# Optimization experiments

Measured on AMD Instinct MI355X. Metric: run time of the kernel, lower is better.

## Reference

```python
import jax, jax.numpy as jnp
import numpy as np

EPS = 1e-4
LN_EPS = 1e-5  # torch LayerNorm default
N, E, IN_DIM, OUT_DIM = 100000, 800000, 128, 128


def setup_inputs() -> dict:
    key = jax.random.key(0)
    ks = jax.random.split(key, 8)
    s = 1.0 / np.sqrt(IN_DIM)
    return {
        "x": jax.random.normal(ks[0], (N, IN_DIM), dtype=jnp.float32),
        "edge_index": jax.random.randint(ks[1], (2, E), 0, N, dtype=jnp.int32),
        "degree": jax.random.randint(ks[2], (N,), 0, 16, dtype=jnp.int32),
        "W_fc": jax.random.normal(ks[3], (IN_DIM, OUT_DIM), dtype=jnp.float32) * s,
        "b_fc": jax.random.normal(ks[4], (OUT_DIM,), dtype=jnp.float32) * s,
        "W_rate": jax.random.normal(ks[5], (IN_DIM, OUT_DIM), dtype=jnp.float32) * s,
        "W_rob": jax.random.normal(ks[6], (IN_DIM, OUT_DIM), dtype=jnp.float32) * s,
        "b_rob": jax.random.normal(ks[7], (OUT_DIM,), dtype=jnp.float32) * s,
        "ln_gamma": jnp.ones((OUT_DIM,), dtype=jnp.float32),
        "ln_beta": jnp.zeros((OUT_DIM,), dtype=jnp.float32),
    }


def reference(x, edge_index, degree, W_fc, b_fc, W_rate, W_rob, b_rob, ln_gamma, ln_beta):
    n = x.shape[0]
    rate = jax.nn.softplus(x @ W_rate) + EPS            # [N, D_out]
    gamma = x @ W_rob + b_rob                           # [N, D_out]
    h = x @ W_fc + b_fc                                 # [N, D_out]
    row, col = edge_index[0], edge_index[1]
    msg = h[row] + h[col]                               # [E, D_out] gather-add
    agg = jax.ops.segment_sum(msg, row, num_segments=n) # scatter_sum over dst
    deg = degree.astype(x.dtype)[:, None]
    y = (rate * agg + gamma) / (1.0 + rate * deg + EPS)
    mean = jnp.mean(y, axis=-1, keepdims=True)
    var = jnp.var(y, axis=-1, keepdims=True)
    y = (y - mean) * jax.lax.rsqrt(var + LN_EPS) * ln_gamma + ln_beta
    return y  # act is Identity
```

## Files before the change

kernel.cpp:

```cpp
#include <hip/hip_runtime.h>
#include <hip/hip_bf16.h>
#include <math.h>

#define NN 100000
#define DIM 128
#define EPSF 1e-4f
#define LN_EPSF 1e-5f
#define XSTR 136
#define NTILES 3125
#define TPB 2
#define GEMM_GRID ((NTILES + TPB - 1) / TPB)
#define PACK_GRID ((NN + 255) / 256)
#define CAP 32

typedef float  floatx4 __attribute__((ext_vector_type(4)));
typedef float  floatx2 __attribute__((ext_vector_type(2)));
typedef short  shortx8 __attribute__((ext_vector_type(8)));

__device__ __forceinline__ ushort f2b(float f) {
    union { float f; unsigned u; } c; c.f = f;
    unsigned lsb = (c.u >> 16) & 1u;
    return (ushort)((c.u + 0x7fffu + lsb) >> 16);
}
__device__ __forceinline__ float b2f(ushort b) {
    union { unsigned u; float f; } c; c.u = ((unsigned)b) << 16;
    return c.f;
}
__device__ __forceinline__ unsigned pk2(float a, float b) {
    union { __hip_bfloat162 h2; unsigned u; } c;
    c.h2 = __float22bfloat162_rn(float2{a, b});
    return c.u;
}

__global__ __launch_bounds__(256) void pack_kernel(
    const float* __restrict__ Wfc, const float* __restrict__ Wrate,
    const float* __restrict__ Wrob, ushort* __restrict__ Bpack,
    int* __restrict__ cur)
{
    const int id = blockIdx.x * 256 + threadIdx.x;
    if (id < NN) cur[id] = 0;
    if (id >= 6144) return;
    const int lane = id & 63;
    const int ks   = (id >> 6) & 3;
    const int nt   = (id >> 8) & 7;
    const int w    = id >> 11;
    const float* W = (w == 0) ? Wfc : (w == 1) ? Wrate : Wrob;
    const int n  = nt * 16 + (lane & 15);
    const int kb = ks * 32 + (lane >> 4) * 8;
    ushort tmp[8];
#pragma unroll
    for (int j = 0; j < 8; ++j) tmp[j] = f2b(W[(kb + j) * DIM + n]);
    ushort* dst = Bpack + (size_t)id * 8;
#pragma unroll
    for (int j = 0; j < 8; ++j) dst[j] = tmp[j];
}

__global__ __launch_bounds__(256) void gemm3_mfma_kernel(
    const float* __restrict__ x,
    const ushort* __restrict__ Bpack,
    const float* __restrict__ bfc, const float* __restrict__ brob,
    ushort* __restrict__ h, ushort* __restrict__ rate, ushort* __restrict__ gam,
    const int* __restrict__ ei, int* __restrict__ cur,
    int* __restrict__ bucket, int E)
{
    __shared__ ushort xs[32 * XSTR];
    __shared__ ushort outb[3 * 32 * XSTR];
    const int tid  = threadIdx.x;
    const int wv   = tid >> 6;
    const int lane = tid & 63;

    for (int e = blockIdx.x * 512 + tid; e < E; e += GEMM_GRID * 512) {
#pragma unroll
        for (int q = 0; q < 2; ++q) {
            const int ee = e + q * 256;
            if (ee < E) {
                const int row = ei[ee];
                const int col = ei[E + ee];
                const int pos = atomicAdd(&cur[row], 1);
                if (pos < CAP) bucket[(size_t)row * CAP + pos] = col;
            }
        }
        break;
    }

    shortx8 bfrag[3][2][4];
#pragma unroll
    for (int w = 0; w < 3; ++w)
#pragma unroll
        for (int t = 0; t < 2; ++t) {
            const int nt = wv * 2 + t;
#pragma unroll
            for (int ks = 0; ks < 4; ++ks) {
                const ushort* p = Bpack + ((((size_t)w * 8 + nt) * 4 + ks) * 64 + lane) * 8;
                bfrag[w][t][ks] = *(const shortx8*)p;
            }
        }

    float4 bias_fc[2], bias_rob[2];
#pragma unroll
    for (int t = 0; t < 2; ++t) {
        const int colbase = wv * 32 + t * 16 + (lane >> 4) * 4;
        bias_fc[t]  = ((const float4*)bfc)[colbase >> 2];
        bias_rob[t] = ((const float4*)brob)[colbase >> 2];
    }

    const int tile0  = blockIdx.x * TPB;
    const int ntiles = (NTILES - tile0 < TPB) ? (NTILES - tile0) : TPB;

    {
        const size_t row0 = (size_t)tile0 * 32;
#pragma unroll
        for (int k = 0; k < 4; ++k) {
            const int i = tid + k * 256, r = i >> 5, c4 = i & 31;
            const float4 v = ((const float4*)(x + (row0 + r) * DIM))[c4];
            uint2 uu; uu.x = pk2(v.x, v.y); uu.y = pk2(v.z, v.w);
            *(uint2*)&xs[r * XSTR + c4 * 4] = uu;
        }
    }
    __syncthreads();

    for (int ti = 0; ti < ntiles; ++ti) {
        const size_t row0 = (size_t)(tile0 + ti) * 32;
        const bool hasnext = (ti + 1 < ntiles);

        float4 pf[4];
        if (hasnext) {
            const size_t nrow0 = row0 + 32;
#pragma unroll
            for (int k = 0; k < 4; ++k) {
                const int i = tid + k * 256, r = i >> 5, c4 = i & 31;
                pf[k] = ((const float4*)(x + (nrow0 + r) * DIM))[c4];
            }
        }

#pragma unroll
        for (int rt = 0; rt < 2; ++rt) {
            shortx8 af[4];
#pragma unroll
            for (int ks = 0; ks < 4; ++ks)
                af[ks] = *(const shortx8*)&xs[(rt * 16 + (lane & 15)) * XSTR
                                              + ks * 32 + (lane >> 4) * 8];
            floatx4 acc[3][2] = {};
#pragma unroll
            for (int ks = 0; ks < 4; ++ks)
#pragma unroll
                for (int w = 0; w < 3; ++w)
#pragma unroll
                    for (int t = 0; t < 2; ++t)
                        acc[w][t] = __builtin_amdgcn_mfma_f32_16x16x32_bf16(
                            bfrag[w][t][ks], af[ks], acc[w][t], 0, 0, 0);

            const int node = rt * 16 + (lane & 15);
#pragma unroll
            for (int t = 0; t < 2; ++t) {
                const int colbase = wv * 32 + t * 16 + (lane >> 4) * 4;
                {
                    uint2 st;
                    st.x = pk2(acc[0][t][0] + bias_fc[t].x, acc[0][t][1] + bias_fc[t].y);
                    st.y = pk2(acc[0][t][2] + bias_fc[t].z, acc[0][t][3] + bias_fc[t].w);
                    *(uint2*)&outb[0 * 32 * XSTR + node * XSTR + colbase] = st;
                }
                {
                    float rv[4];
#pragma unroll
                    for (int r = 0; r < 4; ++r) {
                        const float v = acc[1][t][r];
                        rv[r] = fmaxf(v, 0.f) + __logf(1.f + __expf(-fabsf(v))) + EPSF;
                    }
                    uint2 st; st.x = pk2(rv[0], rv[1]); st.y = pk2(rv[2], rv[3]);
                    *(uint2*)&outb[1 * 32 * XSTR + node * XSTR + colbase] = st;
                }
                {
                    uint2 st;
                    st.x = pk2(acc[2][t][0] + bias_rob[t].x, acc[2][t][1] + bias_rob[t].y);
                    st.y = pk2(acc[2][t][2] + bias_rob[t].z, acc[2][t][3] + bias_rob[t].w);
                    *(uint2*)&outb[2 * 32 * XSTR + node * XSTR + colbase] = st;
                }
            }
        }
        __syncthreads();

#pragma unroll
        for (int k = 0; k < 6; ++k) {
            const int w = k >> 1;
            const int rem = tid + (k & 1) * 256;
            const int node = rem >> 4, seg = rem & 15;
            const uint4 v = *(const uint4*)&outb[w * 32 * XSTR + node * XSTR + seg * 8];
            ushort* dstw = (w == 0) ? h : (w == 1) ? rate : gam;
            *(uint4*)(dstw + (row0 + node) * DIM + seg * 8) = v;
        }

        if (hasnext) {
#pragma unroll
            for (int k = 0; k < 4; ++k) {
                const int i = tid + k * 256, r = i >> 5, c4 = i & 31;
                uint2 uu; uu.x = pk2(pf[k].x, pf[k].y); uu.y = pk2(pf[k].z, pf[k].w);
                *(uint2*)&xs[r * XSTR + c4 * 4] = uu;
            }
        }
        __syncthreads();
    }
}

__global__ __launch_bounds__(256) void finalize_kernel(
    const ushort* __restrict__ h, const ushort* __restrict__ rate,
    const ushort* __restrict__ gam,
    const int* __restrict__ cur, const int* __restrict__ bucket,
    const int* __restrict__ degree,
    const float* __restrict__ ln_g, const float* __restrict__ ln_b,
    float* __restrict__ out)
{
    const int wave = threadIdx.x >> 6;
    const int lane = threadIdx.x & 63;
    const size_t rA = (size_t)blockIdx.x * 8 + wave * 2;
    const size_t rB = rA + 1;
    const unsigned* hu = (const unsigned*)h;

    const int   nA  = cur[rA],            nB  = cur[rB];
    const float dgA = (float)degree[rA],  dgB = (float)degree[rB];
    const int   bvA = bucket[rA * CAP + (lane & 31)];
    const int   bvB = bucket[rB * CAP + (lane & 31)];
    const unsigned hvA = hu[rA * 64 + lane],  hvB = hu[rB * 64 + lane];
    const unsigned rvA = ((const unsigned*)rate)[rA * 64 + lane];
    const unsigned rvB = ((const unsigned*)rate)[rB * 64 + lane];
    const unsigned gvA = ((const unsigned*)gam)[rA * 64 + lane];
    const unsigned gvB = ((const unsigned*)gam)[rB * 64 + lane];
    const float2 lg = ((const float2*)ln_g)[lane];
    const float2 lb = ((const float2*)ln_b)[lane];

    float axA = 0.f, ayA = 0.f, axB = 0.f, ayB = 0.f;
    const int m = (nA < nB) ? nA : nB;
    int j = 0;
    for (; j + 4 <= m; j += 4) {
        int cA[4], cB[4];
#pragma unroll
        for (int q = 0; q < 4; ++q) {
            cA[q] = __shfl(bvA, j + q, 64);
            cB[q] = __shfl(bvB, j + q, 64);
        }
        unsigned vA[4], vB[4];
#pragma unroll
        for (int q = 0; q < 4; ++q) {
            vA[q] = hu[(size_t)cA[q] * 64 + lane];
            vB[q] = hu[(size_t)cB[q] * 64 + lane];
        }
#pragma unroll
        for (int q = 0; q < 4; ++q) {
            axA += b2f((ushort)(vA[q] & 0xffff)); ayA += b2f((ushort)(vA[q] >> 16));
            axB += b2f((ushort)(vB[q] & 0xffff)); ayB += b2f((ushort)(vB[q] >> 16));
        }
    }
    int jA = j;
    for (; jA + 4 <= nA; jA += 4) {
        int c[4]; unsigned v[4];
#pragma unroll
        for (int q = 0; q < 4; ++q) c[q] = __shfl(bvA, jA + q, 64);
#pragma unroll
        for (int q = 0; q < 4; ++q) v[q] = hu[(size_t)c[q] * 64 + lane];
#pragma unroll
        for (int q = 0; q < 4; ++q) {
            axA += b2f((ushort)(v[q] & 0xffff)); ayA += b2f((ushort)(v[q] >> 16));
        }
    }
    for (; jA < nA; ++jA) {
        const unsigned v = hu[(size_t)__shfl(bvA, jA, 64) * 64 + lane];
        axA += b2f((ushort)(v & 0xffff)); ayA += b2f((ushort)(v >> 16));
    }
    int jB = j;
    for (; jB + 4 <= nB; jB += 4) {
        int c[4]; unsigned v[4];
#pragma unroll
        for (int q = 0; q < 4; ++q) c[q] = __shfl(bvB, jB + q, 64);
#pragma unroll
        for (int q = 0; q < 4; ++q) v[q] = hu[(size_t)c[q] * 64 + lane];
#pragma unroll
        for (int q = 0; q < 4; ++q) {
            axB += b2f((ushort)(v[q] & 0xffff)); ayB += b2f((ushort)(v[q] >> 16));
        }
    }
    for (; jB < nB; ++jB) {
        const unsigned v = hu[(size_t)__shfl(bvB, jB, 64) * 64 + lane];
        axB += b2f((ushort)(v & 0xffff)); ayB += b2f((ushort)(v >> 16));
    }

#pragma unroll
    for (int rr = 0; rr < 2; ++rr) {
        const size_t row = rr ? rB : rA;
        const float cn = (float)(rr ? nB : nA);
        const float dg = rr ? dgB : dgA;
        const unsigned hv = rr ? hvB : hvA;
        const unsigned rv = rr ? rvB : rvA;
        const unsigned gv = rr ? gvB : gvA;
        const float ax = rr ? axB : axA, ay = rr ? ayB : ayA;

        const float h0 = b2f((ushort)(hv & 0xffff)), h1 = b2f((ushort)(hv >> 16));
        const float r0 = b2f((ushort)(rv & 0xffff)), r1 = b2f((ushort)(rv >> 16));
        const float g0 = b2f((ushort)(gv & 0xffff)), g1 = b2f((ushort)(gv >> 16));

        const float a0 = cn * h0 + ax;
        const float a1 = cn * h1 + ay;
        const float y0 = (r0 * a0 + g0) / (1.f + r0 * dg + EPSF);
        const float y1 = (r1 * a1 + g1) / (1.f + r1 * dg + EPSF);

        float s  = y0 + y1;
        float s2 = y0 * y0 + y1 * y1;
#pragma unroll
        for (int o = 32; o > 0; o >>= 1) {
            s  += __shfl_xor(s,  o, 64);
            s2 += __shfl_xor(s2, o, 64);
        }
        const float mean = s * (1.f / 128.f);
        const float var  = s2 * (1.f / 128.f) - mean * mean;
        const float inv  = rsqrtf(var + LN_EPSF);

        floatx2 o;
        o.x = (y0 - mean) * inv * lg.x + lb.x;
        o.y = (y1 - mean) * inv * lg.y + lb.y;
        __builtin_nontemporal_store(o, (floatx2*)(out + row * DIM) + lane);
    }
}

extern "C" void kernel_launch(void* const* d_in, const int* in_sizes, int n_in,
                              void* d_out, int out_size, void* d_ws, size_t ws_size,
                              hipStream_t stream)
{
    const float* x      = (const float*)d_in[0];
    const int*   ei     = (const int*)  d_in[1];
    const int*   degree = (const int*)  d_in[2];
    const float* Wfc    = (const float*)d_in[3];
    const float* bfc    = (const float*)d_in[4];
    const float* Wrate  = (const float*)d_in[5];
    const float* Wrob   = (const float*)d_in[6];
    const float* brob   = (const float*)d_in[7];
    const float* ln_g   = (const float*)d_in[8];
    const float* ln_b   = (const float*)d_in[9];
    float* out = (float*)d_out;

    const int E = in_sizes[1] / 2;
    const size_t NEL = (size_t)NN * DIM;

    ushort* h     = (ushort*)d_ws;
    ushort* rate  = h + NEL;
    ushort* gam   = rate + NEL;
    ushort* Bpack = gam + NEL;
    int*   cur    = (int*)(Bpack + 49152);
    int*   bucket = cur + NN;

    pack_kernel<<<PACK_GRID, 256, 0, stream>>>(Wfc, Wrate, Wrob, Bpack, cur);
    gemm3_mfma_kernel<<<GEMM_GRID, 256, 0, stream>>>(x, Bpack, bfc, brob,
                                                     h, rate, gam,
                                                     ei, cur, bucket, E);
    finalize_kernel<<<NN / 8, 256, 0, stream>>>(h, rate, gam, cur, bucket,
                                                degree, ln_g, ln_b, out);
}
```

Baseline: 215.8 us.

## Drop LDS staging in GEMM; load A fragments and store outputs directly

Result: slower. 428.8 us (+98.7%).

```diff
diff --git a/kernel.cpp b/kernel.cpp
--- a/kernel.cpp
+++ b/kernel.cpp
@@ -6,7 +6,6 @@
 #define DIM 128
 #define EPSF 1e-4f
 #define LN_EPSF 1e-5f
-#define XSTR 136
 #define NTILES 3125
 #define TPB 2
 #define GEMM_GRID ((NTILES + TPB - 1) / TPB)
@@ -55,7 +54,7 @@
     for (int j = 0; j < 8; ++j) dst[j] = tmp[j];
 }
 
-__global__ __launch_bounds__(256) void gemm3_mfma_kernel(
+__global__ __launch_bounds__(256, 6) void gemm3_mfma_kernel(
     const float* __restrict__ x,
     const ushort* __restrict__ Bpack,
     const float* __restrict__ bfc, const float* __restrict__ brob,
@@ -63,8 +62,6 @@
     const int* __restrict__ ei, int* __restrict__ cur,
     int* __restrict__ bucket, int E)
 {
-    __shared__ ushort xs[32 * XSTR];
-    __shared__ ushort outb[3 * 32 * XSTR];
     const int tid  = threadIdx.x;
     const int wv   = tid >> 6;
     const int lane = tid & 63;
@@ -107,39 +104,30 @@
     const int tile0  = blockIdx.x * TPB;
     const int ntiles = (NTILES - tile0 < TPB) ? (NTILES - tile0) : TPB;
 
-    {
-        const size_t row0 = (size_t)tile0 * 32;
-#pragma unroll
-        for (int k = 0; k < 4; ++k) {
-            const int i = tid + k * 256, r = i >> 5, c4 = i & 31;
-            const float4 v = ((const float4*)(x + (row0 + r) * DIM))[c4];
-            uint2 uu; uu.x = pk2(v.x, v.y); uu.y = pk2(v.z, v.w);
-            *(uint2*)&xs[r * XSTR + c4 * 4] = uu;
-        }
-    }
-    __syncthreads();
-
     for (int ti = 0; ti < ntiles; ++ti) {
         const size_t row0 = (size_t)(tile0 + ti) * 32;
-        const bool hasnext = (ti + 1 < ntiles);
-
-        float4 pf[4];
-        if (hasnext) {
-            const size_t nrow0 = row0 + 32;
-#pragma unroll
-            for (int k = 0; k < 4; ++k) {
-                const int i = tid + k * 256, r = i >> 5, c4 = i & 31;
-                pf[k] = ((const float4*)(x + (nrow0 + r) * DIM))[c4];
-            }
-        }
 
 #pragma unroll
         for (int rt = 0; rt < 2; ++rt) {
+            const int node = rt * 16 + (lane & 15);
+            const float* xr = x + (row0 + node) * DIM + (lane >> 4) * 8;
+            float4 r0[4], r1[4];
+#pragma unroll
+            for (int ks = 0; ks < 4; ++ks) {
+                r0[ks] = ((const float4*)(xr + ks * 32))[0];
+                r1[ks] = ((const float4*)(xr + ks * 32))[1];
+            }
             shortx8 af[4];
 #pragma unroll
-            for (int ks = 0; ks < 4; ++ks)
-                af[ks] = *(const shortx8*)&xs[(rt * 16 + (lane & 15)) * XSTR
-                                              + ks * 32 + (lane >> 4) * 8];
+            for (int ks = 0; ks < 4; ++ks) {
+                union { shortx8 s; unsigned u[4]; } c;
+                c.u[0] = pk2(r0[ks].x, r0[ks].y);
+                c.u[1] = pk2(r0[ks].z, r0[ks].w);
+                c.u[2] = pk2(r1[ks].x, r1[ks].y);
+                c.u[3] = pk2(r1[ks].z, r1[ks].w);
+                af[ks] = c.s;
+            }
+
             floatx4 acc[3][2] = {};
 #pragma unroll
             for (int ks = 0; ks < 4; ++ks)
@@ -150,7 +138,6 @@
                         acc[w][t] = __builtin_amdgcn_mfma_f32_16x16x32_bf16(
                             bfrag[w][t][ks], af[ks], acc[w][t], 0, 0, 0);
 
-            const int node = rt * 16 + (lane & 15);
 #pragma unroll
             for (int t = 0; t < 2; ++t) {
                 const int colbase = wv * 32 + t * 16 + (lane >> 4) * 4;
@@ -158,7 +145,7 @@
                     uint2 st;
                     st.x = pk2(acc[0][t][0] + bias_fc[t].x, acc[0][t][1] + bias_fc[t].y);
                     st.y = pk2(acc[0][t][2] + bias_fc[t].z, acc[0][t][3] + bias_fc[t].w);
-                    *(uint2*)&outb[0 * 32 * XSTR + node * XSTR + colbase] = st;
+                    *(uint2*)(h + (row0 + node) * DIM + colbase) = st;
                 }
                 {
                     float rv[4];
@@ -168,37 +155,16 @@
                         rv[r] = fmaxf(v, 0.f) + __logf(1.f + __expf(-fabsf(v))) + EPSF;
                     }
                     uint2 st; st.x = pk2(rv[0], rv[1]); st.y = pk2(rv[2], rv[3]);
-                    *(uint2*)&outb[1 * 32 * XSTR + node * XSTR + colbase] = st;
+                    *(uint2*)(rate + (row0 + node) * DIM + colbase) = st;
                 }
                 {
                     uint2 st;
                     st.x = pk2(acc[2][t][0] + bias_rob[t].x, acc[2][t][1] + bias_rob[t].y);
                     st.y = pk2(acc[2][t][2] + bias_rob[t].z, acc[2][t][3] + bias_rob[t].w);
-                    *(uint2*)&outb[2 * 32 * XSTR + node * XSTR + colbase] = st;
+                    *(uint2*)(gam + (row0 + node) * DIM + colbase) = st;
                 }
             }
         }
-        __syncthreads();
-
-#pragma unroll
-        for (int k = 0; k < 6; ++k) {
-            const int w = k >> 1;
-            const int rem = tid + (k & 1) * 256;
-            const int node = rem >> 4, seg = rem & 15;
-            const uint4 v = *(const uint4*)&outb[w * 32 * XSTR + node * XSTR + seg * 8];
-            ushort* dstw = (w == 0) ? h : (w == 1) ? rate : gam;
-            *(uint4*)(dstw + (row0 + node) * DIM + seg * 8) = v;
-        }
-
-        if (hasnext) {
-#pragma unroll
-            for (int k = 0; k < 4; ++k) {
-                const int i = tid + k * 256, r = i >> 5, c4 = i & 31;
-                uint2 uu; uu.x = pk2(pf[k].x, pf[k].y); uu.y = pk2(pf[k].z, pf[k].w);
-                *(uint2*)&xs[r * XSTR + c4 * 4] = uu;
-            }
-        }
-        __syncthreads();
     }
 }
 
```

## Double-buffer x tile in LDS, store GEMM outputs directly, four tiles per block

Applied to the files above, without the earlier changes.

Result: slower. 230.1 us (+6.6%).

```diff
diff --git a/kernel.cpp b/kernel.cpp
--- a/kernel.cpp
+++ b/kernel.cpp
@@ -8,7 +8,7 @@
 #define LN_EPSF 1e-5f
 #define XSTR 136
 #define NTILES 3125
-#define TPB 2
+#define TPB 4
 #define GEMM_GRID ((NTILES + TPB - 1) / TPB)
 #define PACK_GRID ((NN + 255) / 256)
 #define CAP 32
@@ -63,16 +63,17 @@
     const int* __restrict__ ei, int* __restrict__ cur,
     int* __restrict__ bucket, int E)
 {
-    __shared__ ushort xs[32 * XSTR];
-    __shared__ ushort outb[3 * 32 * XSTR];
+    __shared__ ushort xs[2][32 * XSTR];
     const int tid  = threadIdx.x;
     const int wv   = tid >> 6;
     const int lane = tid & 63;
 
-    for (int e = blockIdx.x * 512 + tid; e < E; e += GEMM_GRID * 512) {
-#pragma unroll
-        for (int q = 0; q < 2; ++q) {
-            const int ee = e + q * 256;
+    {
+        const int tcount = GEMM_GRID * 256;
+        const int ebase  = blockIdx.x * 256 + tid;
+#pragma unroll
+        for (int q = 0; q < 4; ++q) {
+            const int ee = ebase + q * tcount;
             if (ee < E) {
                 const int row = ei[ee];
                 const int col = ei[E + ee];
@@ -80,7 +81,12 @@
                 if (pos < CAP) bucket[(size_t)row * CAP + pos] = col;
             }
         }
-        break;
+        for (int ee = ebase + 4 * tcount; ee < E; ee += tcount) {
+            const int row = ei[ee];
+            const int col = ei[E + ee];
+            const int pos = atomicAdd(&cur[row], 1);
+            if (pos < CAP) bucket[(size_t)row * CAP + pos] = col;
+        }
     }
 
     shortx8 bfrag[3][2][4];
@@ -114,7 +120,7 @@
             const int i = tid + k * 256, r = i >> 5, c4 = i & 31;
             const float4 v = ((const float4*)(x + (row0 + r) * DIM))[c4];
             uint2 uu; uu.x = pk2(v.x, v.y); uu.y = pk2(v.z, v.w);
-            *(uint2*)&xs[r * XSTR + c4 * 4] = uu;
+            *(uint2*)&xs[0][r * XSTR + c4 * 4] = uu;
         }
     }
     __syncthreads();
@@ -122,6 +128,7 @@
     for (int ti = 0; ti < ntiles; ++ti) {
         const size_t row0 = (size_t)(tile0 + ti) * 32;
         const bool hasnext = (ti + 1 < ntiles);
+        const int  cb = ti & 1;
 
         float4 pf[4];
         if (hasnext) {
@@ -138,8 +145,8 @@
             shortx8 af[4];
 #pragma unroll
             for (int ks = 0; ks < 4; ++ks)
-                af[ks] = *(const shortx8*)&xs[(rt * 16 + (lane & 15)) * XSTR
-                                              + ks * 32 + (lane >> 4) * 8];
+                af[ks] = *(const shortx8*)&xs[cb][(rt * 16 + (lane & 15)) * XSTR
+                                                  + ks * 32 + (lane >> 4) * 8];
             floatx4 acc[3][2] = {};
 #pragma unroll
             for (int ks = 0; ks < 4; ++ks)
@@ -158,7 +165,7 @@
                     uint2 st;
                     st.x = pk2(acc[0][t][0] + bias_fc[t].x, acc[0][t][1] + bias_fc[t].y);
                     st.y = pk2(acc[0][t][2] + bias_fc[t].z, acc[0][t][3] + bias_fc[t].w);
-                    *(uint2*)&outb[0 * 32 * XSTR + node * XSTR + colbase] = st;
+                    *(uint2*)(h + (row0 + node) * DIM + colbase) = st;
                 }
                 {
                     float rv[4];
@@ -168,26 +175,15 @@
                         rv[r] = fmaxf(v, 0.f) + __logf(1.f + __expf(-fabsf(v))) + EPSF;
                     }
                     uint2 st; st.x = pk2(rv[0], rv[1]); st.y = pk2(rv[2], rv[3]);
-                    *(uint2*)&outb[1 * 32 * XSTR + node * XSTR + colbase] = st;
+                    *(uint2*)(rate + (row0 + node) * DIM + colbase) = st;
                 }
                 {
                     uint2 st;
                     st.x = pk2(acc[2][t][0] + bias_rob[t].x, acc[2][t][1] + bias_rob[t].y);
                     st.y = pk2(acc[2][t][2] + bias_rob[t].z, acc[2][t][3] + bias_rob[t].w);
-                    *(uint2*)&outb[2 * 32 * XSTR + node * XSTR + colbase] = st;
+                    *(uint2*)(gam + (row0 + node) * DIM + colbase) = st;
                 }
             }
-        }
-        __syncthreads();
-
-#pragma unroll
-        for (int k = 0; k < 6; ++k) {
-            const int w = k >> 1;
-            const int rem = tid + (k & 1) * 256;
-            const int node = rem >> 4, seg = rem & 15;
-            const uint4 v = *(const uint4*)&outb[w * 32 * XSTR + node * XSTR + seg * 8];
-            ushort* dstw = (w == 0) ? h : (w == 1) ? rate : gam;
-            *(uint4*)(dstw + (row0 + node) * DIM + seg * 8) = v;
         }
 
         if (hasnext) {
@@ -195,7 +191,7 @@
             for (int k = 0; k < 4; ++k) {
                 const int i = tid + k * 256, r = i >> 5, c4 = i & 31;
                 uint2 uu; uu.x = pk2(pf[k].x, pf[k].y); uu.y = pk2(pf[k].z, pf[k].w);
-                *(uint2*)&xs[r * XSTR + c4 * 4] = uu;
+                *(uint2*)&xs[cb ^ 1][r * XSTR + c4 * 4] = uu;
             }
         }
         __syncthreads();
```
